# Optimization experiments

Measured on AMD Instinct MI355X. Metric: run time of the kernel, lower is better.

Reference implementation:

```python
import jax, jax.numpy as jnp
import numpy as np

H = 2048          # hidden size
NH = 32           # query heads
NKV = 8           # kv heads
HD = H // NH      # head dim = 64
GROUPS = NH // NKV
S = 2048          # seq len
B = 1
SCALE = HD ** -0.5


def _rope_tables(seq, dim, base=10000.0):
    inv = 1.0 / (base ** (np.arange(0, dim, 2, dtype=np.float32) / dim))
    t = np.arange(seq, dtype=np.float32)
    freqs = np.outer(t, inv)                     # [S, dim/2]
    emb = np.concatenate([freqs, freqs], axis=-1)  # [S, dim]
    return jnp.asarray(np.cos(emb)), jnp.asarray(np.sin(emb))


def setup_inputs() -> dict:
    key = jax.random.key(0)
    ks = jax.random.split(key, 5)
    x = jax.random.normal(ks[0], (B, S, H), dtype=jnp.float32)
    wq = jax.random.normal(ks[1], (H, NH * HD), dtype=jnp.float32) * (H ** -0.5)
    wk = jax.random.normal(ks[2], (H, NKV * HD), dtype=jnp.float32) * (H ** -0.5)
    wv = jax.random.normal(ks[3], (H, NKV * HD), dtype=jnp.float32) * (H ** -0.5)
    wo = jax.random.normal(ks[4], (NH * HD, H), dtype=jnp.float32) * (H ** -0.5)
    cos, sin = _rope_tables(S, HD)
    mask = jnp.tril(jnp.ones((S, S), dtype=bool))[None, None]  # causal [1,1,S,S]
    return {"x": x, "wq": wq, "wk": wk, "wv": wv, "wo": wo,
            "cos": cos, "sin": sin, "mask": mask}


def _rotate_half(t):
    t1, t2 = jnp.split(t, 2, axis=-1)
    return jnp.concatenate([-t2, t1], axis=-1)


def reference(x, wq, wk, wv, wo, cos, sin, mask):
    b, s, _ = x.shape
    # projections
    q = (x @ wq).reshape(b, s, NH, HD).transpose(0, 2, 1, 3)    # [B,NH,S,HD]
    k = (x @ wk).reshape(b, s, NKV, HD).transpose(0, 2, 1, 3)   # [B,NKV,S,HD]
    v = (x @ wv).reshape(b, s, NKV, HD).transpose(0, 2, 1, 3)
    # RoPE (cos/sin broadcast over batch and heads)
    c = cos[None, None]; sn = sin[None, None]
    q = q * c + _rotate_half(q) * sn
    k = k * c + _rotate_half(k) * sn
    # GQA: repeat kv heads to match query heads
    k = jnp.repeat(k, GROUPS, axis=1)                           # [B,NH,S,HD]
    v = jnp.repeat(v, GROUPS, axis=1)
    # scores + causal mask + softmax (dropout p=0 -> identity in eval)
    scores = SCALE * jnp.einsum('bhqd,bhkd->bhqk', q, k)
    scores = jnp.where(mask, scores, -jnp.inf)
    attn = jax.nn.softmax(scores, axis=-1)
    out = jnp.einsum('bhqk,bhkd->bhqd', attn, v)
    out = out.transpose(0, 2, 1, 3).reshape(b, s, NH * HD)
    return out @ wo
```

## Files before the change

### kernel.cpp

```cpp
#include <hip/hip_runtime.h>

typedef unsigned short u16;
typedef unsigned u32;
typedef u16 u16x8 __attribute__((ext_vector_type(8)));
typedef u16 u16x4 __attribute__((ext_vector_type(4)));
typedef u32 u32x4 __attribute__((ext_vector_type(4)));
typedef __bf16 bf8 __attribute__((ext_vector_type(8)));
typedef float f32x4 __attribute__((ext_vector_type(4)));
typedef float f32x16 __attribute__((ext_vector_type(16)));

__device__ __forceinline__ u16 f2b(float f) {
  unsigned u = __float_as_uint(f);
  u += 0x7FFFu + ((u >> 16) & 1u);
  return (u16)(u >> 16);
}
__device__ __forceinline__ float b2f(u16 h) {
  return __uint_as_float(((unsigned)h) << 16);
}
__device__ __forceinline__ bf8 asbf8(u16x8 v) {
  return __builtin_bit_cast(bf8, v);
}
__device__ __forceinline__ void gll16(const u16* g, u16* l) {
  __builtin_amdgcn_global_load_lds(
      (const __attribute__((address_space(1))) unsigned*)(g),
      (__attribute__((address_space(3))) unsigned*)(l), 16, 0, 0);
}
__device__ __forceinline__ u32 cvtpk(float lo, float hi) {
  u32 r;
  asm("v_cvt_pk_bf16_f32 %0, %1, %2" : "=v"(r) : "v"(lo), "v"(hi));
  return r;
}
__device__ __forceinline__ void plswap(u32& a, u32& b) {
  asm("v_permlane32_swap_b32 %0, %1" : "+v"(a), "+v"(b));
}
__device__ __forceinline__ float max3f(float a, float b, float c) {
  float r;
  asm("v_max3_f32 %0, %1, %2, %3" : "=v"(r) : "v"(a), "v"(b), "v"(c));
  return r;
}
__device__ __forceinline__ float ex2(float x) {
  return __builtin_amdgcn_exp2f(x);
}


__global__ __launch_bounds__(256) void xconv(const float* __restrict__ x,
                                             u16* __restrict__ xb) {
  int i = (blockIdx.x * 256 + threadIdx.x) * 4;
  float4 v = *(const float4*)(x + i);
  u16x4 o;
  o[0] = f2b(v.x); o[1] = f2b(v.y); o[2] = f2b(v.z); o[3] = f2b(v.w);
  *(u16x4*)(xb + i) = o;
}

__global__ __launch_bounds__(256) void wtrans(const float* __restrict__ in,
                                              u16* __restrict__ out,
                                              int N, int K) {
  __shared__ float tile[32][33];
  int tx = threadIdx.x & 31, ty = threadIdx.x >> 5;
  int n0 = blockIdx.x * 32, k0 = blockIdx.y * 32;
#pragma unroll
  for (int yy = 0; yy < 32; yy += 8)
    tile[ty + yy][tx] = in[(size_t)(k0 + ty + yy) * N + n0 + tx];
  __syncthreads();
#pragma unroll
  for (int yy = 0; yy < 32; yy += 8)
    out[(size_t)(n0 + ty + yy) * K + k0 + tx] = f2b(tile[tx][ty + yy]);
}

__global__ __launch_bounds__(256) void reduce_qkv(u16* __restrict__ p0,
                                                  const u16* __restrict__ p1,
                                                  const float* __restrict__ cs,
                                                  const float* __restrict__ sn) {
  int idx = blockIdx.x * 256 + threadIdx.x;
  int s = idx / 384, c8 = (idx % 384) * 8;
  size_t base = (size_t)s * 3072 + c8;
  if (c8 < 2560) {
    int hc = c8 & 63;
    if (hc >= 32) return;
    u16x8 a0 = *(const u16x8*)(p0 + base);
    u16x8 a1 = *(const u16x8*)(p1 + base);
    u16x8 b0 = *(const u16x8*)(p0 + base + 32);
    u16x8 b1 = *(const u16x8*)(p1 + base + 32);
    u16x8 oa, ob;
#pragma unroll
    for (int e = 0; e < 8; ++e) {
      float va = b2f(a0[e]) + b2f(a1[e]);
      float vb = b2f(b0[e]) + b2f(b1[e]);
      float c1 = cs[s * 64 + hc + e],      s1 = sn[s * 64 + hc + e];
      float c2 = cs[s * 64 + hc + 32 + e], s2 = sn[s * 64 + hc + 32 + e];
      oa[e] = f2b(va * c1 - vb * s1);
      ob[e] = f2b(vb * c2 + va * s2);
    }
    *(u16x8*)(p0 + base)      = oa;
    *(u16x8*)(p0 + base + 32) = ob;
  } else {
    u16x8 a0 = *(const u16x8*)(p0 + base);
    u16x8 a1 = *(const u16x8*)(p1 + base);
    u16x8 o;
#pragma unroll
    for (int e = 0; e < 8; ++e) o[e] = f2b(b2f(a0[e]) + b2f(a1[e]));
    *(u16x8*)(p0 + base) = o;
  }
}

__global__ __launch_bounds__(256) void reduce_out(const u16* __restrict__ p0,
                                                  const u16* __restrict__ p1,
                                                  float* __restrict__ out) {
  int idx = blockIdx.x * 256 + threadIdx.x;
  size_t base = (size_t)idx * 8;
  u16x8 a0 = *(const u16x8*)(p0 + base);
  u16x8 a1 = *(const u16x8*)(p1 + base);
  float4 lo, hi;
  lo.x = b2f(a0[0]) + b2f(a1[0]); lo.y = b2f(a0[1]) + b2f(a1[1]);
  lo.z = b2f(a0[2]) + b2f(a1[2]); lo.w = b2f(a0[3]) + b2f(a1[3]);
  hi.x = b2f(a0[4]) + b2f(a1[4]); hi.y = b2f(a0[5]) + b2f(a1[5]);
  hi.z = b2f(a0[6]) + b2f(a1[6]); hi.w = b2f(a0[7]) + b2f(a1[7]);
  *(float4*)(out + base)     = lo;
  *(float4*)(out + base + 4) = hi;
}

__global__ __launch_bounds__(256) void ktrans_f(const u16* __restrict__ qkv,
                                                u16* __restrict__ Kf) {
  int tid = blockIdx.x * 256 + threadIdx.x;
  int s = tid >> 6, cc = tid & 63;
  int kh = cc >> 3, c = cc & 7;
  int j = c >> 1, hi = c & 1;
  int b = s >> 5, la = s & 31;
  u16x8 v = *(const u16x8*)(qkv + (size_t)s * 3072 + 2048 + cc * 8);
  *(u16x8*)(Kf + ((((size_t)(kh * 64 + b) * 4 + j) * 2 + hi) * 32 + la) * 8) = v;
}

__global__ __launch_bounds__(256) void vtrans_f(const u16* __restrict__ qkv,
                                                u16* __restrict__ Vf) {
  int tid = blockIdx.x * 256 + threadIdx.x;
  int s = tid >> 6, cc = tid & 63;
  int kh = cc >> 3, c = cc & 7;
  int m = c >> 2, laB = (c & 3) * 8;
  int b = s >> 5, s5 = s & 31;
  int jj = s5 >> 4, hi = (s5 >> 3) & 1, e = s5 & 7;
  u16x8 v = *(const u16x8*)(qkv + (size_t)s * 3072 + 2560 + cc * 8);
  u16* dst = Vf + (((size_t)(kh * 64 + b) * 4 + m * 2 + jj) * 64 + hi * 32 + laB) * 8 + e;
#pragma unroll
  for (int i = 0; i < 8; ++i) dst[i * 8] = v[i];
}


__global__ __launch_bounds__(256) void gemm_sk(const u16* __restrict__ A,
                                               const u16* __restrict__ Bt,
                                               u16* __restrict__ C0,
                                               u16* __restrict__ C1,
                                               int N, int Kfull, int KH) {
  __shared__ __align__(16) u16 As[128 * 32];
  __shared__ __align__(16) u16 Bs[128 * 32];
  const int t = threadIdx.x;
  const int lane = t & 63, wid = t >> 6;
  const int wm = (wid >> 1) * 64, wn = (wid & 1) * 64;
  const int la = lane & 15, lg = lane >> 4;
  const int m0 = blockIdx.y * 128, n0 = blockIdx.x * 128;
  const int kbeg = blockIdx.z * KH;
  u16* C = blockIdx.z ? C1 : C0;

  const int c0 = wid * 2;
  const int srow = c0 * 16 + (lane >> 2);
  const int scol = (lane & 3) * 8;
  const u16* Ap = A + (size_t)(m0 + srow) * Kfull + kbeg + scol;
  const u16* Bp = Bt + (size_t)(n0 + srow) * Kfull + kbeg + scol;
  u16* Ad0 = &As[c0 * 512];
  u16* Ad1 = &As[(c0 + 1) * 512];
  u16* Bd0 = &Bs[c0 * 512];
  u16* Bd1 = &Bs[(c0 + 1) * 512];
  const size_t rstep = (size_t)16 * Kfull;

  f32x4 acc[4][4] = {};

  for (int k0 = 0; k0 < KH; k0 += 32) {
    __syncthreads();
    gll16(Ap + k0, Ad0);
    gll16(Ap + k0 + rstep, Ad1);
    gll16(Bp + k0, Bd0);
    gll16(Bp + k0 + rstep, Bd1);
    __syncthreads();
    bf8 af[4], bfr[4];
#pragma unroll
    for (int i = 0; i < 4; ++i)
      af[i] = asbf8(*(const u16x8*)(&As[(wm + i * 16 + la) * 32 + lg * 8]));
#pragma unroll
    for (int j = 0; j < 4; ++j)
      bfr[j] = asbf8(*(const u16x8*)(&Bs[(wn + j * 16 + la) * 32 + lg * 8]));
    __builtin_amdgcn_s_setprio(1);
#pragma unroll
    for (int i = 0; i < 4; ++i)
#pragma unroll
      for (int j = 0; j < 4; ++j)
        acc[i][j] = __builtin_amdgcn_mfma_f32_16x16x32_bf16(af[i], bfr[j],
                                                            acc[i][j], 0, 0, 0);
    __builtin_amdgcn_s_setprio(0);
  }

#pragma unroll
  for (int i = 0; i < 4; ++i)
#pragma unroll
    for (int j = 0; j < 4; ++j)
#pragma unroll
      for (int r = 0; r < 4; ++r) {
        int row = m0 + wm + i * 16 + lg * 4 + r;
        int col = n0 + wn + j * 16 + la;
        C[(size_t)row * N + col] = f2b(acc[i][j][r]);
      }
}


#define LOADKV(K0,K1,K2,K3,V0,V1,V2,V3,b) do {                       \
    const u16* kp_ = kfb + (size_t)(b) * 2048;                       \
    K0 = asbf8(*(const u16x8*)(kp_));                                \
    K1 = asbf8(*(const u16x8*)(kp_ + 512));                          \
    K2 = asbf8(*(const u16x8*)(kp_ + 1024));                         \
    K3 = asbf8(*(const u16x8*)(kp_ + 1536));                         \
    const u16* vp_ = vfb + (size_t)(b) * 2048;                       \
    V0 = asbf8(*(const u16x8*)(vp_));                                \
    V1 = asbf8(*(const u16x8*)(vp_ + 512));                          \
    V2 = asbf8(*(const u16x8*)(vp_ + 1024));                         \
    V3 = asbf8(*(const u16x8*)(vp_ + 1536));                         \
  } while (0)

#define QKMAX(K0,K1,K2,K3,b) \
    f32x16 s = {};                                                   \
    __builtin_amdgcn_s_setprio(1);                                   \
    s = __builtin_amdgcn_mfma_f32_32x32x16_bf16(K0, qf0, s, 0, 0, 0);\
    s = __builtin_amdgcn_mfma_f32_32x32x16_bf16(K1, qf1, s, 0, 0, 0);\
    s = __builtin_amdgcn_mfma_f32_32x32x16_bf16(K2, qf2, s, 0, 0, 0);\
    s = __builtin_amdgcn_mfma_f32_32x32x16_bf16(K3, qf3, s, 0, 0, 0);\
    __builtin_amdgcn_s_setprio(0);                                   \
    if ((b) == nb - 1) {                                             \
      _Pragma("unroll") for (int r = 0; r < 16; ++r) {               \
        int kvr = (b) * 32 + (r & 3) + 8 * (r >> 2) + 4 * hi;        \
        if (kvr > q0w + la) s[r] = -1e30f;                           \
      }                                                              \
    }                                                                \
    float pmax = fmaxf(                                              \
        max3f(max3f(s[0], s[1], s[2]),  max3f(s[3], s[4], s[5]),     \
              max3f(s[6], s[7], s[8])),                              \
        max3f(max3f(s[9], s[10], s[11]),                             \
              max3f(s[12], s[13], s[14]), s[15]));

#define EXPPV(V0,V1,V2,V3) do {                                      \
    _Pragma("unroll") for (int r = 0; r < 16; ++r)                   \
      s[r] = ex2(s[r] - m_run);                                      \
    float z0 = s[0] + s[1],   z1 = s[2] + s[3];                      \
    float z2 = s[4] + s[5],   z3 = s[6] + s[7];                      \
    float z4 = s[8] + s[9],   z5 = s[10] + s[11];                    \
    float z6 = s[12] + s[13], z7 = s[14] + s[15];                    \
    float w0 = z0 + z1, w1 = z2 + z3, w2 = z4 + z5, w3 = z6 + z7;    \
    l_run += (w0 + w1) + (w2 + w3);                                  \
    u32 c0 = cvtpk(s[0], s[1]),   c1 = cvtpk(s[2], s[3]);            \
    u32 c2 = cvtpk(s[4], s[5]),   c3 = cvtpk(s[6], s[7]);            \
    u32 c4 = cvtpk(s[8], s[9]),   c5 = cvtpk(s[10], s[11]);          \
    u32 c6 = cvtpk(s[12], s[13]), c7 = cvtpk(s[14], s[15]);          \
    plswap(c0, c2); plswap(c1, c3); plswap(c4, c6); plswap(c5, c7);  \
    u32x4 t0; t0[0] = c0; t0[1] = c1; t0[2] = c2; t0[3] = c3;        \
    u32x4 t1; t1[0] = c4; t1[1] = c5; t1[2] = c6; t1[3] = c7;        \
    bf8 pa0 = __builtin_bit_cast(bf8, t0);                           \
    bf8 pa1 = __builtin_bit_cast(bf8, t1);                           \
    __builtin_amdgcn_s_setprio(1);                                   \
    o0 = __builtin_amdgcn_mfma_f32_32x32x16_bf16(pa0, V0, o0, 0, 0, 0);\
    o0 = __builtin_amdgcn_mfma_f32_32x32x16_bf16(pa1, V1, o0, 0, 0, 0);\
    o1 = __builtin_amdgcn_mfma_f32_32x32x16_bf16(pa0, V2, o1, 0, 0, 0);\
    o1 = __builtin_amdgcn_mfma_f32_32x32x16_bf16(pa1, V3, o1, 0, 0, 0);\
    __builtin_amdgcn_s_setprio(0);                                   \
  } while (0)

#define STEP1(K0,K1,K2,K3,V0,V1,V2,V3,b) do {                        \
    QKMAX(K0,K1,K2,K3,b)                                             \
    float om = __shfl_xor(pmax, 32);                                 \
    m_run = fmaxf(pmax, om);                                         \
    EXPPV(V0,V1,V2,V3);                                              \
  } while (0)

#define STEP(K0,K1,K2,K3,V0,V1,V2,V3,b) do {                         \
    QKMAX(K0,K1,K2,K3,b)                                             \
    if (!__all(pmax - m_run <= 8.0f)) {                              \
      float om = __shfl_xor(pmax, 32);                               \
      float mn = fmaxf(m_run, fmaxf(pmax, om));                      \
      float sc = ex2(m_run - mn);                                    \
      m_run = mn; l_run *= sc;                                       \
      _Pragma("unroll") for (int r = 0; r < 16; ++r) {               \
        float scr = __shfl(sc, (r & 3) + 8 * (r >> 2) + 4 * hi);     \
        o0[r] *= scr; o1[r] *= scr;                                  \
      }                                                              \
    }                                                                \
    EXPPV(V0,V1,V2,V3);                                              \
  } while (0)

__global__ __launch_bounds__(256) void attn_fwd(const u16* __restrict__ qkv,
                                                const u16* __restrict__ Kf,
                                                const u16* __restrict__ Vf,
                                                u16* __restrict__ aout) {
  const int head = blockIdx.x;
  const int qt = 63 - (int)blockIdx.y;
  const int nb = qt + 1;
  const int q0w = qt * 32;
  const int kh = head >> 2;
  const int t = threadIdx.x;
  const int w = t >> 6;
  const int lane = t & 63;
  const int la = lane & 31;
  const int hi = lane >> 5;

  __shared__ float mL[4][32];
  __shared__ float lL[4][32];
  __shared__ __align__(16) u16 oL[4][32][72];

  const int base = nb >> 2, rem = nb & 3;
  const int cnt = base + (w < rem);
  const int start = w * base + min(w, rem);

  bf8 qf0, qf1, qf2, qf3;
  {
    const u16* qp = qkv + (size_t)(q0w + la) * 3072 + head * 64 + hi * 8;
    const float SC = 0.125f * 1.44269504088896340736f;
#define QLOAD(dst, kk) do {                                          \
      u16x8 v = *(const u16x8*)(qp + (kk) * 16);                     \
      u16x8 sv;                                                      \
      _Pragma("unroll") for (int e = 0; e < 8; ++e)                  \
        sv[e] = f2b(b2f(v[e]) * SC);                                 \
      dst = asbf8(sv);                                               \
    } while (0)
    QLOAD(qf0, 0); QLOAD(qf1, 1); QLOAD(qf2, 2); QLOAD(qf3, 3);
#undef QLOAD
  }

  const u16* kfb = Kf + (size_t)kh * 131072 + (size_t)lane * 8;
  const u16* vfb = Vf + (size_t)kh * 131072 + (size_t)lane * 8;

  f32x16 o0 = {}, o1 = {};
  float m_run = -1e30f, l_run = 0.f;

  bf8 kA0, kA1, kA2, kA3, vA0, vA1, vA2, vA3;
  bf8 kB0, kB1, kB2, kB3, vB0, vB1, vB2, vB3;

  if (cnt > 0) {
    int b = start;
    const int e = start + cnt;
    LOADKV(kA0, kA1, kA2, kA3, vA0, vA1, vA2, vA3, b);
    if (b + 1 < e) LOADKV(kB0, kB1, kB2, kB3, vB0, vB1, vB2, vB3, b + 1);
    STEP1(kA0, kA1, kA2, kA3, vA0, vA1, vA2, vA3, b);
    ++b;
    while (b < e) {
      if (b + 1 < e) LOADKV(kA0, kA1, kA2, kA3, vA0, vA1, vA2, vA3, b + 1);
      STEP(kB0, kB1, kB2, kB3, vB0, vB1, vB2, vB3, b);
      ++b; if (b >= e) break;
      if (b + 1 < e) LOADKV(kB0, kB1, kB2, kB3, vB0, vB1, vB2, vB3, b + 1);
      STEP(kA0, kA1, kA2, kA3, vA0, vA1, vA2, vA3, b);
      ++b;
    }
  }

  {
    float lt = l_run + __shfl_xor(l_run, 32);
    if (lane < 32) { mL[w][lane] = m_run; lL[w][lane] = lt; }
#pragma unroll
    for (int r = 0; r < 16; ++r) {
      int crow = (r & 3) + 8 * (r >> 2) + 4 * hi;
      oL[w][crow][la]      = f2b(o0[r]);
      oL[w][crow][la + 32] = f2b(o1[r]);
    }
  }
  __syncthreads();

  {
    const int q = t >> 3, d0 = (t & 7) * 8;
    float m0_ = mL[0][q], m1_ = mL[1][q], m2_ = mL[2][q], m3_ = mL[3][q];
    float mg = fmaxf(fmaxf(m0_, m1_), fmaxf(m2_, m3_));
    float s0 = ex2(m0_ - mg), s1 = ex2(m1_ - mg);
    float s2 = ex2(m2_ - mg), s3 = ex2(m3_ - mg);
    float lg = s0 * lL[0][q] + s1 * lL[1][q] + s2 * lL[2][q] + s3 * lL[3][q];
    float inv = 1.0f / lg;
    u16x8 p0 = *(const u16x8*)&oL[0][q][d0];
    u16x8 p1 = *(const u16x8*)&oL[1][q][d0];
    u16x8 p2 = *(const u16x8*)&oL[2][q][d0];
    u16x8 p3 = *(const u16x8*)&oL[3][q][d0];
    u16x8 outv;
#pragma unroll
    for (int j = 0; j < 8; ++j) {
      float sum = s0 * b2f(p0[j]) + s1 * b2f(p1[j]) +
                  s2 * b2f(p2[j]) + s3 * b2f(p3[j]);
      outv[j] = f2b(sum * inv);
    }
    *(u16x8*)(aout + (size_t)(q0w + q) * 2048 + head * 64 + d0) = outv;
  }
}


extern "C" void kernel_launch(void* const* d_in, const int* in_sizes, int n_in,
                              void* d_out, int out_size, void* d_ws, size_t ws_size,
                              hipStream_t stream) {
  (void)in_sizes; (void)n_in; (void)out_size; (void)ws_size;
  const float* x  = (const float*)d_in[0];
  const float* wq = (const float*)d_in[1];
  const float* wk = (const float*)d_in[2];
  const float* wv = (const float*)d_in[3];
  const float* wo = (const float*)d_in[4];
  const float* cs = (const float*)d_in[5];
  const float* sn = (const float*)d_in[6];

  u16* ws    = (u16*)d_ws;
  u16* xb    = ws;
  u16* wqkvT = ws + 4194304;
  u16* qkv   = ws + 10485760;
  u16* woT   = ws + 16777216;
  u16* ext   = ws + 20971520;
  u16* Kf    = wqkvT;
  u16* Vf    = wqkvT + 1048576;
  u16* aout  = xb;
  u16* op0   = qkv;
  u16* op1   = ext;

  xconv<<<4096, 256, 0, stream>>>(x, xb);
  wtrans<<<dim3(64, 64), 256, 0, stream>>>(wq, wqkvT, 2048, 2048);
  wtrans<<<dim3(16, 64), 256, 0, stream>>>(wk, wqkvT + (size_t)2048 * 2048, 512, 2048);
  wtrans<<<dim3(16, 64), 256, 0, stream>>>(wv, wqkvT + (size_t)2560 * 2048, 512, 2048);
  wtrans<<<dim3(64, 64), 256, 0, stream>>>(wo, woT, 2048, 2048);

  gemm_sk<<<dim3(24, 16, 2), 256, 0, stream>>>(xb, wqkvT, qkv, ext, 3072, 2048, 1024);
  reduce_qkv<<<3072, 256, 0, stream>>>(qkv, ext, cs, sn);
  ktrans_f<<<512, 256, 0, stream>>>(qkv, Kf);
  vtrans_f<<<512, 256, 0, stream>>>(qkv, Vf);
  attn_fwd<<<dim3(32, 64), 256, 0, stream>>>(qkv, Kf, Vf, aout);
  gemm_sk<<<dim3(16, 16, 2), 256, 0, stream>>>(aout, woT, op0, op1, 2048, 2048, 1024);
  reduce_out<<<2048, 256, 0, stream>>>(op0, op1, (float*)d_out);
}
```

Measured before the change: 155.5 us.

## Process 64 query rows per attention block to reuse K/V fragments

Result: slower. 165.7 us (+6.5%).

```diff
diff --git a/kernel.cpp b/kernel.cpp
--- a/kernel.cpp
+++ b/kernel.cpp
@@ -41,6 +41,7 @@
 __device__ __forceinline__ float ex2(float x) {
   return __builtin_amdgcn_exp2f(x);
 }
+#define MFMA32(A,B,C) __builtin_amdgcn_mfma_f32_32x32x16_bf16(A,B,C,0,0,0)
 
 
 __global__ __launch_bounds__(256) void xconv(const float* __restrict__ x,
@@ -223,72 +224,107 @@
     V3 = asbf8(*(const u16x8*)(vp_ + 1536));                         \
   } while (0)
 
-#define QKMAX(K0,K1,K2,K3,b) \
-    f32x16 s = {};                                                   \
+#define QKMAX2(K0,K1,K2,K3,b)                                        \
+    f32x16 sL = {}, sH = {};                                         \
     __builtin_amdgcn_s_setprio(1);                                   \
-    s = __builtin_amdgcn_mfma_f32_32x32x16_bf16(K0, qf0, s, 0, 0, 0);\
-    s = __builtin_amdgcn_mfma_f32_32x32x16_bf16(K1, qf1, s, 0, 0, 0);\
-    s = __builtin_amdgcn_mfma_f32_32x32x16_bf16(K2, qf2, s, 0, 0, 0);\
-    s = __builtin_amdgcn_mfma_f32_32x32x16_bf16(K3, qf3, s, 0, 0, 0);\
+    sL = MFMA32(K0, qfL0, sL); sH = MFMA32(K0, qfH0, sH);            \
+    sL = MFMA32(K1, qfL1, sL); sH = MFMA32(K1, qfH1, sH);            \
+    sL = MFMA32(K2, qfL2, sL); sH = MFMA32(K2, qfH2, sH);            \
+    sL = MFMA32(K3, qfL3, sL); sH = MFMA32(K3, qfH3, sH);            \
     __builtin_amdgcn_s_setprio(0);                                   \
-    if ((b) == nb - 1) {                                             \
+    if ((b) >= nb - 2) {                                             \
       _Pragma("unroll") for (int r = 0; r < 16; ++r) {               \
         int kvr = (b) * 32 + (r & 3) + 8 * (r >> 2) + 4 * hi;        \
-        if (kvr > q0w + la) s[r] = -1e30f;                           \
+        if (kvr > q0w + la) sL[r] = -1e30f;                          \
+        if (kvr > q0w + 32 + la) sH[r] = -1e30f;                     \
       }                                                              \
     }                                                                \
-    float pmax = fmaxf(                                              \
-        max3f(max3f(s[0], s[1], s[2]),  max3f(s[3], s[4], s[5]),     \
-              max3f(s[6], s[7], s[8])),                              \
-        max3f(max3f(s[9], s[10], s[11]),                             \
-              max3f(s[12], s[13], s[14]), s[15]));
-
-#define EXPPV(V0,V1,V2,V3) do {                                      \
+    float pmL = fmaxf(                                               \
+        max3f(max3f(sL[0], sL[1], sL[2]),  max3f(sL[3], sL[4], sL[5]),\
+              max3f(sL[6], sL[7], sL[8])),                           \
+        max3f(max3f(sL[9], sL[10], sL[11]),                          \
+              max3f(sL[12], sL[13], sL[14]), sL[15]));               \
+    float pmH = fmaxf(                                               \
+        max3f(max3f(sH[0], sH[1], sH[2]),  max3f(sH[3], sH[4], sH[5]),\
+              max3f(sH[6], sH[7], sH[8])),                           \
+        max3f(max3f(sH[9], sH[10], sH[11]),                          \
+              max3f(sH[12], sH[13], sH[14]), sH[15]));
+
+#define EXPPV2(V0,V1,V2,V3) do {                                     \
     _Pragma("unroll") for (int r = 0; r < 16; ++r)                   \
-      s[r] = ex2(s[r] - m_run);                                      \
-    float z0 = s[0] + s[1],   z1 = s[2] + s[3];                      \
-    float z2 = s[4] + s[5],   z3 = s[6] + s[7];                      \
-    float z4 = s[8] + s[9],   z5 = s[10] + s[11];                    \
-    float z6 = s[12] + s[13], z7 = s[14] + s[15];                    \
-    float w0 = z0 + z1, w1 = z2 + z3, w2 = z4 + z5, w3 = z6 + z7;    \
-    l_run += (w0 + w1) + (w2 + w3);                                  \
-    u32 c0 = cvtpk(s[0], s[1]),   c1 = cvtpk(s[2], s[3]);            \
-    u32 c2 = cvtpk(s[4], s[5]),   c3 = cvtpk(s[6], s[7]);            \
-    u32 c4 = cvtpk(s[8], s[9]),   c5 = cvtpk(s[10], s[11]);          \
-    u32 c6 = cvtpk(s[12], s[13]), c7 = cvtpk(s[14], s[15]);          \
-    plswap(c0, c2); plswap(c1, c3); plswap(c4, c6); plswap(c5, c7);  \
-    u32x4 t0; t0[0] = c0; t0[1] = c1; t0[2] = c2; t0[3] = c3;        \
-    u32x4 t1; t1[0] = c4; t1[1] = c5; t1[2] = c6; t1[3] = c7;        \
-    bf8 pa0 = __builtin_bit_cast(bf8, t0);                           \
-    bf8 pa1 = __builtin_bit_cast(bf8, t1);                           \
+      sL[r] = ex2(sL[r] - mrL);                                      \
+    _Pragma("unroll") for (int r = 0; r < 16; ++r)                   \
+      sH[r] = ex2(sH[r] - mrH);                                      \
+    {                                                                \
+      float z0 = sL[0]+sL[1], z1 = sL[2]+sL[3], z2 = sL[4]+sL[5];    \
+      float z3 = sL[6]+sL[7], z4 = sL[8]+sL[9], z5 = sL[10]+sL[11];  \
+      float z6 = sL[12]+sL[13], z7 = sL[14]+sL[15];                  \
+      lrL += ((z0+z1)+(z2+z3)) + ((z4+z5)+(z6+z7));                  \
+    }                                                                \
+    {                                                                \
+      float z0 = sH[0]+sH[1], z1 = sH[2]+sH[3], z2 = sH[4]+sH[5];    \
+      float z3 = sH[6]+sH[7], z4 = sH[8]+sH[9], z5 = sH[10]+sH[11];  \
+      float z6 = sH[12]+sH[13], z7 = sH[14]+sH[15];                  \
+      lrH += ((z0+z1)+(z2+z3)) + ((z4+z5)+(z6+z7));                  \
+    }                                                                \
+    u32 cL0 = cvtpk(sL[0],sL[1]),   cL1 = cvtpk(sL[2],sL[3]);        \
+    u32 cL2 = cvtpk(sL[4],sL[5]),   cL3 = cvtpk(sL[6],sL[7]);        \
+    u32 cL4 = cvtpk(sL[8],sL[9]),   cL5 = cvtpk(sL[10],sL[11]);      \
+    u32 cL6 = cvtpk(sL[12],sL[13]), cL7 = cvtpk(sL[14],sL[15]);      \
+    plswap(cL0,cL2); plswap(cL1,cL3); plswap(cL4,cL6); plswap(cL5,cL7);\
+    u32 cH0 = cvtpk(sH[0],sH[1]),   cH1 = cvtpk(sH[2],sH[3]);        \
+    u32 cH2 = cvtpk(sH[4],sH[5]),   cH3 = cvtpk(sH[6],sH[7]);        \
+    u32 cH4 = cvtpk(sH[8],sH[9]),   cH5 = cvtpk(sH[10],sH[11]);      \
+    u32 cH6 = cvtpk(sH[12],sH[13]), cH7 = cvtpk(sH[14],sH[15]);      \
+    plswap(cH0,cH2); plswap(cH1,cH3); plswap(cH4,cH6); plswap(cH5,cH7);\
+    u32x4 tl0; tl0[0]=cL0; tl0[1]=cL1; tl0[2]=cL2; tl0[3]=cL3;       \
+    u32x4 tl1; tl1[0]=cL4; tl1[1]=cL5; tl1[2]=cL6; tl1[3]=cL7;       \
+    u32x4 th0; th0[0]=cH0; th0[1]=cH1; th0[2]=cH2; th0[3]=cH3;       \
+    u32x4 th1; th1[0]=cH4; th1[1]=cH5; th1[2]=cH6; th1[3]=cH7;       \
+    bf8 paL0 = __builtin_bit_cast(bf8, tl0);                         \
+    bf8 paL1 = __builtin_bit_cast(bf8, tl1);                         \
+    bf8 paH0 = __builtin_bit_cast(bf8, th0);                         \
+    bf8 paH1 = __builtin_bit_cast(bf8, th1);                         \
     __builtin_amdgcn_s_setprio(1);                                   \
-    o0 = __builtin_amdgcn_mfma_f32_32x32x16_bf16(pa0, V0, o0, 0, 0, 0);\
-    o0 = __builtin_amdgcn_mfma_f32_32x32x16_bf16(pa1, V1, o0, 0, 0, 0);\
-    o1 = __builtin_amdgcn_mfma_f32_32x32x16_bf16(pa0, V2, o1, 0, 0, 0);\
-    o1 = __builtin_amdgcn_mfma_f32_32x32x16_bf16(pa1, V3, o1, 0, 0, 0);\
+    ol0 = MFMA32(paL0, V0, ol0); oh0 = MFMA32(paH0, V0, oh0);        \
+    ol0 = MFMA32(paL1, V1, ol0); oh0 = MFMA32(paH1, V1, oh0);        \
+    ol1 = MFMA32(paL0, V2, ol1); oh1 = MFMA32(paH0, V2, oh1);        \
+    ol1 = MFMA32(paL1, V3, ol1); oh1 = MFMA32(paH1, V3, oh1);        \
     __builtin_amdgcn_s_setprio(0);                                   \
   } while (0)
 
 #define STEP1(K0,K1,K2,K3,V0,V1,V2,V3,b) do {                        \
-    QKMAX(K0,K1,K2,K3,b)                                             \
-    float om = __shfl_xor(pmax, 32);                                 \
-    m_run = fmaxf(pmax, om);                                         \
-    EXPPV(V0,V1,V2,V3);                                              \
+    QKMAX2(K0,K1,K2,K3,b)                                            \
+    float omL = __shfl_xor(pmL, 32);                                 \
+    mrL = fmaxf(pmL, omL);                                           \
+    float omH = __shfl_xor(pmH, 32);                                 \
+    mrH = fmaxf(pmH, omH);                                           \
+    EXPPV2(V0,V1,V2,V3);                                             \
   } while (0)
 
 #define STEP(K0,K1,K2,K3,V0,V1,V2,V3,b) do {                         \
-    QKMAX(K0,K1,K2,K3,b)                                             \
-    if (!__all(pmax - m_run <= 8.0f)) {                              \
-      float om = __shfl_xor(pmax, 32);                               \
-      float mn = fmaxf(m_run, fmaxf(pmax, om));                      \
-      float sc = ex2(m_run - mn);                                    \
-      m_run = mn; l_run *= sc;                                       \
+    QKMAX2(K0,K1,K2,K3,b)                                            \
+    if (!__all(pmL - mrL <= 8.0f)) {                                 \
+      float omL = __shfl_xor(pmL, 32);                               \
+      float mnL = fmaxf(mrL, fmaxf(pmL, omL));                       \
+      float scL = ex2(mrL - mnL);                                    \
+      mrL = mnL; lrL *= scL;                                         \
       _Pragma("unroll") for (int r = 0; r < 16; ++r) {               \
-        float scr = __shfl(sc, (r & 3) + 8 * (r >> 2) + 4 * hi);     \
-        o0[r] *= scr; o1[r] *= scr;                                  \
+        float scr = __shfl(scL, (r & 3) + 8 * (r >> 2) + 4 * hi);    \
+        ol0[r] *= scr; ol1[r] *= scr;                                \
       }                                                              \
     }                                                                \
-    EXPPV(V0,V1,V2,V3);                                              \
+    if (!__all(pmH - mrH <= 8.0f)) {                                 \
+      float omH = __shfl_xor(pmH, 32);                               \
+      float mnH = fmaxf(mrH, fmaxf(pmH, omH));                       \
+      float scH = ex2(mrH - mnH);                                    \
+      mrH = mnH; lrH *= scH;                                         \
+      _Pragma("unroll") for (int r = 0; r < 16; ++r) {               \
+        float scr = __shfl(scH, (r & 3) + 8 * (r >> 2) + 4 * hi);    \
+        oh0[r] *= scr; oh1[r] *= scr;                                \
+      }                                                              \
+    }                                                                \
+    EXPPV2(V0,V1,V2,V3);                                             \
   } while (0)
 
 __global__ __launch_bounds__(256) void attn_fwd(const u16* __restrict__ qkv,
@@ -296,9 +332,9 @@
                                                 const u16* __restrict__ Vf,
                                                 u16* __restrict__ aout) {
   const int head = blockIdx.x;
-  const int qt = 63 - (int)blockIdx.y;
-  const int nb = qt + 1;
-  const int q0w = qt * 32;
+  const int qt = 31 - (int)blockIdx.y;
+  const int nb = 2 * qt + 2;
+  const int q0w = qt * 64;
   const int kh = head >> 2;
   const int t = threadIdx.x;
   const int w = t >> 6;
@@ -306,34 +342,38 @@
   const int la = lane & 31;
   const int hi = lane >> 5;
 
-  __shared__ float mL[4][32];
-  __shared__ float lL[4][32];
-  __shared__ __align__(16) u16 oL[4][32][72];
+  __shared__ float mS[4][64];
+  __shared__ float lS[4][64];
+  __shared__ __align__(16) u16 oS[4][64][72];
 
   const int base = nb >> 2, rem = nb & 3;
   const int cnt = base + (w < rem);
   const int start = w * base + min(w, rem);
 
-  bf8 qf0, qf1, qf2, qf3;
+  bf8 qfL0, qfL1, qfL2, qfL3, qfH0, qfH1, qfH2, qfH3;
   {
-    const u16* qp = qkv + (size_t)(q0w + la) * 3072 + head * 64 + hi * 8;
     const float SC = 0.125f * 1.44269504088896340736f;
-#define QLOAD(dst, kk) do {                                          \
-      u16x8 v = *(const u16x8*)(qp + (kk) * 16);                     \
+    const u16* qpL = qkv + (size_t)(q0w + la) * 3072 + head * 64 + hi * 8;
+    const u16* qpH = qpL + (size_t)32 * 3072;
+#define QLOAD(dst, qp, kk) do {                                      \
+      u16x8 v = *(const u16x8*)((qp) + (kk) * 16);                   \
       u16x8 sv;                                                      \
       _Pragma("unroll") for (int e = 0; e < 8; ++e)                  \
         sv[e] = f2b(b2f(v[e]) * SC);                                 \
       dst = asbf8(sv);                                               \
     } while (0)
-    QLOAD(qf0, 0); QLOAD(qf1, 1); QLOAD(qf2, 2); QLOAD(qf3, 3);
+    QLOAD(qfL0, qpL, 0); QLOAD(qfL1, qpL, 1);
+    QLOAD(qfL2, qpL, 2); QLOAD(qfL3, qpL, 3);
+    QLOAD(qfH0, qpH, 0); QLOAD(qfH1, qpH, 1);
+    QLOAD(qfH2, qpH, 2); QLOAD(qfH3, qpH, 3);
 #undef QLOAD
   }
 
   const u16* kfb = Kf + (size_t)kh * 131072 + (size_t)lane * 8;
   const u16* vfb = Vf + (size_t)kh * 131072 + (size_t)lane * 8;
 
-  f32x16 o0 = {}, o1 = {};
-  float m_run = -1e30f, l_run = 0.f;
+  f32x16 ol0 = {}, ol1 = {}, oh0 = {}, oh1 = {};
+  float mrL = -1e30f, lrL = 0.f, mrH = -1e30f, lrH = 0.f;
 
   bf8 kA0, kA1, kA2, kA3, vA0, vA1, vA2, vA3;
   bf8 kB0, kB1, kB2, kB3, vB0, vB1, vB2, vB3;
@@ -356,29 +396,37 @@
   }
 
   {
-    float lt = l_run + __shfl_xor(l_run, 32);
-    if (lane < 32) { mL[w][lane] = m_run; lL[w][lane] = lt; }
+    float ltL = lrL + __shfl_xor(lrL, 32);
+    float ltH = lrH + __shfl_xor(lrH, 32);
+    if (lane < 32) {
+      mS[w][lane] = mrL;      lS[w][lane] = ltL;
+      mS[w][lane + 32] = mrH; lS[w][lane + 32] = ltH;
+    }
 #pragma unroll
     for (int r = 0; r < 16; ++r) {
       int crow = (r & 3) + 8 * (r >> 2) + 4 * hi;
-      oL[w][crow][la]      = f2b(o0[r]);
-      oL[w][crow][la + 32] = f2b(o1[r]);
+      oS[w][crow][la]           = f2b(ol0[r]);
+      oS[w][crow][la + 32]      = f2b(ol1[r]);
+      oS[w][crow + 32][la]      = f2b(oh0[r]);
+      oS[w][crow + 32][la + 32] = f2b(oh1[r]);
     }
   }
   __syncthreads();
 
-  {
-    const int q = t >> 3, d0 = (t & 7) * 8;
-    float m0_ = mL[0][q], m1_ = mL[1][q], m2_ = mL[2][q], m3_ = mL[3][q];
+#pragma unroll
+  for (int it = 0; it < 2; ++it) {
+    const int id = t + it * 256;
+    const int q = id >> 3, d0 = (id & 7) * 8;
+    float m0_ = mS[0][q], m1_ = mS[1][q], m2_ = mS[2][q], m3_ = mS[3][q];
     float mg = fmaxf(fmaxf(m0_, m1_), fmaxf(m2_, m3_));
     float s0 = ex2(m0_ - mg), s1 = ex2(m1_ - mg);
     float s2 = ex2(m2_ - mg), s3 = ex2(m3_ - mg);
-    float lg = s0 * lL[0][q] + s1 * lL[1][q] + s2 * lL[2][q] + s3 * lL[3][q];
+    float lg = s0 * lS[0][q] + s1 * lS[1][q] + s2 * lS[2][q] + s3 * lS[3][q];
     float inv = 1.0f / lg;
-    u16x8 p0 = *(const u16x8*)&oL[0][q][d0];
-    u16x8 p1 = *(const u16x8*)&oL[1][q][d0];
-    u16x8 p2 = *(const u16x8*)&oL[2][q][d0];
-    u16x8 p3 = *(const u16x8*)&oL[3][q][d0];
+    u16x8 p0 = *(const u16x8*)&oS[0][q][d0];
+    u16x8 p1 = *(const u16x8*)&oS[1][q][d0];
+    u16x8 p2 = *(const u16x8*)&oS[2][q][d0];
+    u16x8 p3 = *(const u16x8*)&oS[3][q][d0];
     u16x8 outv;
 #pragma unroll
     for (int j = 0; j < 8; ++j) {
@@ -425,7 +473,7 @@
   reduce_qkv<<<3072, 256, 0, stream>>>(qkv, ext, cs, sn);
   ktrans_f<<<512, 256, 0, stream>>>(qkv, Kf);
   vtrans_f<<<512, 256, 0, stream>>>(qkv, Vf);
-  attn_fwd<<<dim3(32, 64), 256, 0, stream>>>(qkv, Kf, Vf, aout);
+  attn_fwd<<<dim3(32, 32), 256, 0, stream>>>(qkv, Kf, Vf, aout);
   gemm_sk<<<dim3(16, 16, 2), 256, 0, stream>>>(aout, woT, op0, op1, 2048, 2048, 1024);
   reduce_out<<<2048, 256, 0, stream>>>(op0, op1, (float*)d_out);
 }
```
